# Kernel optimization log

Hardware: AMD Instinct MI355X
Metric: run time of the kernel (lower is better)

Reference implementation:

```python
import jax, jax.numpy as jnp
import numpy as np

N_NODES = 50000
N_EDGES = 800000
D_IN = 128
D_OUT = 128


def setup_inputs() -> dict:
    key = jax.random.key(0)
    k1, k2, k3, k4, k5, k6 = jax.random.split(key, 6)
    x = jax.random.normal(k1, (N_NODES, D_IN), dtype=jnp.float32)
    weight = jax.random.normal(k2, (D_IN, D_OUT), dtype=jnp.float32)
    bias = jax.random.normal(k3, (D_OUT,), dtype=jnp.float32)
    adj_row = jax.random.randint(k4, (N_EDGES,), 0, N_NODES, dtype=jnp.int64)
    adj_col = jax.random.randint(k5, (N_EDGES,), 0, N_NODES, dtype=jnp.int64)
    adj_val = jax.random.uniform(k6, (N_EDGES,), dtype=jnp.float32)
    return {"x": x, "weight": weight, "bias": bias,
            "adj_row": adj_row, "adj_col": adj_col, "adj_val": adj_val}


def reference(x, weight, bias, adj_row, adj_col, adj_val):
    # support = x @ W  -- dense GEMM [N, D_in] x [D_in, D_out]
    support = jnp.matmul(x, weight)
    # spmm(adj, support): out[i] = sum_e adj_val[e] * support[adj_col[e]] for adj_row[e]==i
    messages = support[adj_col] * adj_val[:, None]          # [E, D_out]
    output = jax.ops.segment_sum(messages, adj_row, num_segments=x.shape[0])
    return output + bias
```

## Files before the change

kernel.cpp:

```cpp
#include <hip/hip_runtime.h>

#define D 128
#define RPB 64
#define RPB_SHIFT 6
#define EPT 8
#define CHUNK (256 * EPT)
#define PASS_EDGES 1280

typedef __attribute__((ext_vector_type(8))) short short8;
typedef __attribute__((ext_vector_type(4))) float floatx4;
typedef __attribute__((ext_vector_type(4))) float f32x4;
typedef __attribute__((ext_vector_type(2))) unsigned int u32x2;
typedef unsigned int uint;
typedef unsigned short ushort;

__device__ inline short f2bf(float f) {
  unsigned u = __float_as_uint(f);
  u += 0x7FFF + ((u >> 16) & 1);
  return (short)(u >> 16);
}

__global__ __launch_bounds__(256) void hist_wconv_kernel(
    const int* __restrict__ adj_row, int* __restrict__ counts,
    int n_edges, int nb, int nc,
    const float* __restrict__ w, ushort* __restrict__ wt) {
  __shared__ int hist[1024];
  const int tid = threadIdx.x;

  if ((int)blockIdx.x < nc) {
    const int c = blockIdx.x;
    for (int i = tid; i < nb; i += 256) hist[i] = 0;
    __syncthreads();
    const int base = c * CHUNK + tid * EPT;
    if (base + EPT <= n_edges) {
      int4 r0 = *(const int4*)&adj_row[base];
      int4 r1 = *(const int4*)&adj_row[base + 4];
      int rr[EPT] = {r0.x, r0.y, r0.z, r0.w, r1.x, r1.y, r1.z, r1.w};
#pragma unroll
      for (int u = 0; u < EPT; ++u) atomicAdd(&hist[rr[u] >> RPB_SHIFT], 1);
    } else {
      for (int u = 0; u < EPT; ++u) {
        int e = base + u;
        if (e < n_edges) atomicAdd(&hist[adj_row[e] >> RPB_SHIFT], 1);
      }
    }
    __syncthreads();
    for (int b = tid; b < nb; b += 256)
      counts[(size_t)b * nc + c] = hist[b];
  } else {
    const int idx = ((int)blockIdx.x - nc) * 256 + tid;
    const int m = idx >> 4;
    const int ks = (idx & 15) * 8;
    short8 frag;
#pragma unroll
    for (int j = 0; j < 8; ++j) frag[j] = f2bf(w[(ks + j) * D + m]);
    *(short8*)&wt[(size_t)m * D + ks] = frag;
  }
}

__global__ __launch_bounds__(256) void scan_chunks_kernel(int* __restrict__ counts,
                                                          int* __restrict__ tot,
                                                          int nb, int nc) {
  __shared__ int buf[512];
  const int b = blockIdx.x;
  const int t = threadIdx.x;
  int v0 = (t < nc) ? counts[(size_t)b * nc + t] : 0;
  int v1 = (256 + t < nc) ? counts[(size_t)b * nc + 256 + t] : 0;
  buf[t] = v0;
  buf[256 + t] = v1;
  __syncthreads();
  for (int off = 1; off < 512; off <<= 1) {
    int a0 = buf[t], a1 = buf[256 + t];
    int d0 = (t >= off) ? buf[t - off] : 0;
    int d1 = (256 + t >= off) ? buf[256 + t - off] : 0;
    __syncthreads();
    buf[t] = a0 + d0;
    buf[256 + t] = a1 + d1;
    __syncthreads();
  }
  if (t < nc) counts[(size_t)b * nc + t] = buf[t] - v0;
  if (256 + t < nc) counts[(size_t)b * nc + 256 + t] = buf[256 + t] - v1;
  if (t == 0) tot[b] = buf[511];
}

__global__ __launch_bounds__(256) void scan_bins_kernel(const int* __restrict__ tot,
                                                        int* __restrict__ binStart,
                                                        int nb) {
  __shared__ int buf[1024];
  const int t = threadIdx.x;
  for (int i = t; i < 1024; i += 256) buf[i] = (i < nb) ? tot[i] : 0;
  __syncthreads();
  for (int off = 1; off < 1024; off <<= 1) {
    int a[4], d[4];
#pragma unroll
    for (int k = 0; k < 4; ++k) {
      int i = t + 256 * k;
      a[k] = buf[i];
      d[k] = (i >= off) ? buf[i - off] : 0;
    }
    __syncthreads();
#pragma unroll
    for (int k = 0; k < 4; ++k) buf[t + 256 * k] = a[k] + d[k];
    __syncthreads();
  }
  for (int i = t; i < nb; i += 256) binStart[i] = buf[i] - tot[i];
  if (t == 0) binStart[nb] = buf[1023];
}

__global__ __launch_bounds__(256) void gemm_sort_kernel(
    const float* __restrict__ x, const ushort* __restrict__ wt,
    ushort* __restrict__ support, int n_nodes, int gemm_blocks,
    const int* __restrict__ adj_row, const int* __restrict__ adj_col,
    const float* __restrict__ adj_val, const int* __restrict__ rel,
    const int* __restrict__ binStart, uint2* __restrict__ sorted,
    int n_edges, int nb, int nc) {
  __shared__ short sWA[2 * 8 * 64 * 8];
  const int tid = threadIdx.x;

  if ((int)blockIdx.x < gemm_blocks) {
    const int wid = tid >> 6;
    const int lane = tid & 63;
    const int quad = lane >> 4;
    const int node = blockIdx.x * 64 + wid * 16 + (lane & 15);
    const bool ok = (node < n_nodes);

    floatx4 acc[8];
#pragma unroll
    for (int mt = 0; mt < 8; ++mt) acc[mt] = (floatx4){0.f, 0.f, 0.f, 0.f};

#pragma unroll
    for (int kt2 = 0; kt2 < 4; kt2 += 2) {
      if (kt2) __syncthreads();
      for (int s = tid; s < 1024; s += 256) {
        int ktmt = s >> 6, ls = s & 63;
        int kt = kt2 + (ktmt >> 3);
        int kb = kt * 32 + (ls >> 4) * 8;
        int m = (ktmt & 7) * 16 + (ls & 15);
        *(short8*)&sWA[s * 8] = *(const short8*)&wt[(size_t)m * D + kb];
      }
      __syncthreads();

#pragma unroll
      for (int ktoff = 0; ktoff < 2; ++ktoff) {
        const int kt = kt2 + ktoff;
        short8 bfr = (short8){0, 0, 0, 0, 0, 0, 0, 0};
        if (ok) {
          const float4 v0 = *(const float4*)&x[(size_t)node * D + kt * 32 + quad * 8];
          const float4 v1 = *(const float4*)&x[(size_t)node * D + kt * 32 + quad * 8 + 4];
          bfr = (short8){f2bf(v0.x), f2bf(v0.y), f2bf(v0.z), f2bf(v0.w),
                         f2bf(v1.x), f2bf(v1.y), f2bf(v1.z), f2bf(v1.w)};
        }
#pragma unroll
        for (int mt = 0; mt < 8; ++mt) {
          short8 a = *(const short8*)&sWA[((ktoff * 8 + mt) * 64 + lane) * 8];
          acc[mt] = __builtin_amdgcn_mfma_f32_16x16x32_bf16(a, bfr, acc[mt], 0, 0, 0);
        }
      }
    }

    if (ok) {
#pragma unroll
      for (int mt = 0; mt < 8; ++mt) {
        uint lo = ((uint)(ushort)f2bf(acc[mt][1]) << 16) | (ushort)f2bf(acc[mt][0]);
        uint hi = ((uint)(ushort)f2bf(acc[mt][3]) << 16) | (ushort)f2bf(acc[mt][2]);
        *(uint2*)&support[(size_t)node * D + mt * 16 + quad * 4] = make_uint2(lo, hi);
      }
    }
  } else {
    int* loff = (int*)sWA;
    const int c = (int)blockIdx.x - gemm_blocks;
    for (int i = tid; i < nb; i += 256)
      loff[i] = binStart[i] + rel[(size_t)i * nc + c];
    __syncthreads();

    const int base = c * CHUNK + tid * EPT;
    if (base + EPT <= n_edges) {
      int4 r0 = *(const int4*)&adj_row[base];
      int4 r1 = *(const int4*)&adj_row[base + 4];
      int4 c0 = *(const int4*)&adj_col[base];
      int4 c1 = *(const int4*)&adj_col[base + 4];
      float4 v0 = *(const float4*)&adj_val[base];
      float4 v1 = *(const float4*)&adj_val[base + 4];
      int rr[EPT] = {r0.x, r0.y, r0.z, r0.w, r1.x, r1.y, r1.z, r1.w};
      int cc[EPT] = {c0.x, c0.y, c0.z, c0.w, c1.x, c1.y, c1.z, c1.w};
      float vv[EPT] = {v0.x, v0.y, v0.z, v0.w, v1.x, v1.y, v1.z, v1.w};
#pragma unroll
      for (int u = 0; u < EPT; ++u) {
        int r = rr[u];
        int pos = atomicAdd(&loff[r >> RPB_SHIFT], 1);
        sorted[pos] = make_uint2(((uint)(r & (RPB - 1)) << 16) | (uint)cc[u],
                                 __float_as_uint(vv[u]));
      }
    } else {
      for (int u = 0; u < EPT; ++u) {
        int e = base + u;
        if (e >= n_edges) break;
        int r = adj_row[e];
        int pos = atomicAdd(&loff[r >> RPB_SHIFT], 1);
        sorted[pos] = make_uint2(((uint)(r & (RPB - 1)) << 16) | (uint)adj_col[e],
                                 __float_as_uint(adj_val[e]));
      }
    }
  }
}

#define FMA8(vv, sv, IT)                                                  \
  do {                                                                    \
    acc[IT][0] = fmaf(vv, __uint_as_float((sv).x << 16), acc[IT][0]);     \
    acc[IT][1] = fmaf(vv, __uint_as_float((sv).x & 0xffff0000u), acc[IT][1]); \
    acc[IT][2] = fmaf(vv, __uint_as_float((sv).y << 16), acc[IT][2]);     \
    acc[IT][3] = fmaf(vv, __uint_as_float((sv).y & 0xffff0000u), acc[IT][3]); \
    acc[IT][4] = fmaf(vv, __uint_as_float((sv).z << 16), acc[IT][4]);     \
    acc[IT][5] = fmaf(vv, __uint_as_float((sv).z & 0xffff0000u), acc[IT][5]); \
    acc[IT][6] = fmaf(vv, __uint_as_float((sv).w << 16), acc[IT][6]);     \
    acc[IT][7] = fmaf(vv, __uint_as_float((sv).w & 0xffff0000u), acc[IT][7]); \
  } while (0)

__global__ __launch_bounds__(256) void bin_spmm_kernel(
    const uint2* __restrict__ sorted, const int* __restrict__ binStart,
    const uint* __restrict__ sup, const float* __restrict__ bias,
    float* __restrict__ out, int n_nodes) {
  __shared__ uint2 ebuf[PASS_EDGES];
  __shared__ int rowStart[RPB + 1];
  __shared__ int cursor[RPB];
  const int b = blockIdx.x;
  const int t = threadIdx.x;
  const int wid = t >> 6;
  const int lane = t & 63;
  const int qtr = lane >> 4;
  const int hl = lane & 15;

  const int s0 = binStart[b], s1 = binStart[b + 1];

  float acc[4][8];
#pragma unroll
  for (int it = 0; it < 4; ++it)
#pragma unroll
    for (int k = 0; k < 8; ++k) acc[it][k] = 0.f;

  for (int p0 = s0; p0 < s1; p0 += PASS_EDGES) {
    const int cntp = min(PASS_EDGES, s1 - p0);
    __syncthreads();
    if (t < RPB) cursor[t] = 0;
    __syncthreads();

    u32x2 er[8];
    int rr[8];
    const int base = p0 + t * EPT;
#pragma unroll
    for (int u = 0; u < EPT; ++u) {
      if (t * EPT + u < cntp) {
        er[u] = __builtin_nontemporal_load(
            (const u32x2*)&sorted[base + u]);
        rr[u] = (int)(er[u][0] >> 16);
        atomicAdd(&cursor[rr[u]], 1);
      } else {
        er[u] = (u32x2){0u, 0u};
        rr[u] = -1;
      }
    }
    __syncthreads();

    if (wid == 0) {
      int v = cursor[lane];
      int inc = v;
#pragma unroll
      for (int off = 1; off < 64; off <<= 1) {
        int u = __shfl_up(inc, off);
        if (lane >= off) inc += u;
      }
      rowStart[lane] = inc - v;
      if (lane == 63) rowStart[RPB] = inc;
    }
    __syncthreads();
    if (t < RPB) cursor[t] = rowStart[t];
    __syncthreads();

#pragma unroll
    for (int u = 0; u < EPT; ++u) {
      if (rr[u] >= 0) {
        int pos = atomicAdd(&cursor[rr[u]], 1);
        ebuf[pos] = make_uint2(er[u][0] & 0xFFFFu, er[u][1]);
      }
    }
    __syncthreads();

#pragma unroll
    for (int it = 0; it < 4; ++it) {
      const int rid = it * 16 + wid * 4 + qtr;
      const int js = rowStart[rid], je = rowStart[rid + 1];
      int j = js;
      for (; j + 8 <= je; j += 8) {
        uint cols[8];
        float vs[8];
#pragma unroll
        for (int u = 0; u < 8; ++u) {
          uint2 e = ebuf[j + u];
          cols[u] = e.x;
          vs[u] = __uint_as_float(e.y);
        }
        uint4 sv[8];
#pragma unroll
        for (int u = 0; u < 8; ++u)
          sv[u] = *(const uint4*)&sup[(size_t)cols[u] * 64 + hl * 4];
#pragma unroll
        for (int u = 0; u < 8; ++u) FMA8(vs[u], sv[u], it);
      }
      for (; j + 4 <= je; j += 4) {
        uint cols[4];
        float vs[4];
#pragma unroll
        for (int u = 0; u < 4; ++u) {
          uint2 e = ebuf[j + u];
          cols[u] = e.x;
          vs[u] = __uint_as_float(e.y);
        }
        uint4 sv[4];
#pragma unroll
        for (int u = 0; u < 4; ++u)
          sv[u] = *(const uint4*)&sup[(size_t)cols[u] * 64 + hl * 4];
#pragma unroll
        for (int u = 0; u < 4; ++u) FMA8(vs[u], sv[u], it);
      }
      for (; j < je; ++j) {
        uint2 e = ebuf[j];
        uint4 sv = *(const uint4*)&sup[(size_t)e.x * 64 + hl * 4];
        float v = __uint_as_float(e.y);
        FMA8(v, sv, it);
      }
    }
  }

  float4 b0 = *(const float4*)&bias[hl * 8];
  float4 b1 = *(const float4*)&bias[hl * 8 + 4];
#pragma unroll
  for (int it = 0; it < 4; ++it) {
    const int rid = it * 16 + wid * 4 + qtr;
    const int row = b * RPB + rid;
    if (row < n_nodes) {
      f32x4 o0 = {acc[it][0] + b0.x, acc[it][1] + b0.y,
                  acc[it][2] + b0.z, acc[it][3] + b0.w};
      f32x4 o1 = {acc[it][4] + b1.x, acc[it][5] + b1.y,
                  acc[it][6] + b1.z, acc[it][7] + b1.w};
      __builtin_nontemporal_store(o0, (f32x4*)&out[(size_t)row * D + hl * 8]);
      __builtin_nontemporal_store(o1, (f32x4*)&out[(size_t)row * D + hl * 8 + 4]);
    }
  }
}

extern "C" void kernel_launch(void* const* d_in, const int* in_sizes, int n_in,
                              void* d_out, int out_size, void* d_ws, size_t ws_size,
                              hipStream_t stream) {
  const float* x       = (const float*)d_in[0];
  const float* w       = (const float*)d_in[1];
  const float* bias    = (const float*)d_in[2];
  const int*   adj_row = (const int*)d_in[3];
  const int*   adj_col = (const int*)d_in[4];
  const float* adj_val = (const float*)d_in[5];

  const int n_nodes = in_sizes[0] / D;
  const int n_edges = in_sizes[3];
  float* out = (float*)d_out;

  const int nb = (n_nodes + RPB - 1) / RPB;
  const int nc = (n_edges + CHUNK - 1) / CHUNK;
  const int gemm_blocks = (n_nodes + 63) / 64;

  char* ws = (char*)d_ws;
  ushort* support  = (ushort*)ws; ws += ((size_t)n_nodes * D * 2 + 15) & ~15ull;
  int*    counts   = (int*)ws;    ws += ((size_t)nb * nc * 4 + 15) & ~15ull;
  int*    tot      = (int*)ws;    ws += ((size_t)nb * 4 + 15) & ~15ull;
  int*    binStart = (int*)ws;    ws += ((size_t)(nb + 1) * 4 + 15) & ~15ull;
  ushort* wt       = (ushort*)ws; ws += (size_t)D * D * 2;
  uint2*  sorted   = (uint2*)ws;  ws += (size_t)n_edges * 8;

  hist_wconv_kernel<<<nc + 8, 256, 0, stream>>>(adj_row, counts, n_edges, nb, nc,
                                                w, wt);

  scan_chunks_kernel<<<nb, 256, 0, stream>>>(counts, tot, nb, nc);

  scan_bins_kernel<<<1, 256, 0, stream>>>(tot, binStart, nb);

  gemm_sort_kernel<<<gemm_blocks + nc, 256, 0, stream>>>(
      x, wt, support, n_nodes, gemm_blocks,
      adj_row, adj_col, adj_val, counts, binStart, sorted, n_edges, nb, nc);

  bin_spmm_kernel<<<nb, 256, 0, stream>>>(sorted, binStart, (const uint*)support,
                                          bias, out, n_nodes);
}
```

Baseline: 142.4 us.

## Fuse bin scan into chunk scan via last-block atomic; load full W tile once

Removes the separate single-block scan_bins launch by having the last finishing scan_chunks block, detected with an atomic counter plus thread fences, perform the bin-total scan. The counter is reset inside the histogram kernel. The GEMM path now stages all four K-slices of the bf16 weight into shared memory in one pass, dropping the intermediate __syncthreads. This doubles LDS use per block, which may lower occupancy. The change trades one kernel launch for fence and atomic overhead.

```diff
diff --git a/kernel.cpp b/kernel.cpp
--- a/kernel.cpp
+++ b/kernel.cpp
@@ -6,6 +6,7 @@
 #define EPT 8
 #define CHUNK (256 * EPT)
 #define PASS_EDGES 1280
+#define NBMAX 1024
 
 typedef __attribute__((ext_vector_type(8))) short short8;
 typedef __attribute__((ext_vector_type(4))) float floatx4;
@@ -23,8 +24,9 @@
 __global__ __launch_bounds__(256) void hist_wconv_kernel(
     const int* __restrict__ adj_row, int* __restrict__ counts,
     int n_edges, int nb, int nc,
-    const float* __restrict__ w, ushort* __restrict__ wt) {
-  __shared__ int hist[1024];
+    const float* __restrict__ w, ushort* __restrict__ wt,
+    int* __restrict__ scanflag) {
+  __shared__ int hist[NBMAX];
   const int tid = threadIdx.x;
 
   if ((int)blockIdx.x < nc) {
@@ -49,6 +51,7 @@
       counts[(size_t)b * nc + c] = hist[b];
   } else {
     const int idx = ((int)blockIdx.x - nc) * 256 + tid;
+    if (idx == 0) *scanflag = 0;
     const int m = idx >> 4;
     const int ks = (idx & 15) * 8;
     short8 frag;
@@ -58,10 +61,12 @@
   }
 }
 
-__global__ __launch_bounds__(256) void scan_chunks_kernel(int* __restrict__ counts,
-                                                          int* __restrict__ tot,
-                                                          int nb, int nc) {
-  __shared__ int buf[512];
+__global__ __launch_bounds__(256) void scan_chunks_kernel(
+    int* __restrict__ counts, int* __restrict__ tot,
+    int* __restrict__ binStart, int* __restrict__ scanflag,
+    int nb, int nc) {
+  __shared__ int buf[NBMAX];
+  __shared__ int amLast;
   const int b = blockIdx.x;
   const int t = threadIdx.x;
   int v0 = (t < nc) ? counts[(size_t)b * nc + t] : 0;
@@ -81,16 +86,17 @@
   if (t < nc) counts[(size_t)b * nc + t] = buf[t] - v0;
   if (256 + t < nc) counts[(size_t)b * nc + 256 + t] = buf[256 + t] - v1;
   if (t == 0) tot[b] = buf[511];
-}
-
-__global__ __launch_bounds__(256) void scan_bins_kernel(const int* __restrict__ tot,
-                                                        int* __restrict__ binStart,
-                                                        int nb) {
-  __shared__ int buf[1024];
-  const int t = threadIdx.x;
-  for (int i = t; i < 1024; i += 256) buf[i] = (i < nb) ? tot[i] : 0;
+
+  __threadfence();
   __syncthreads();
-  for (int off = 1; off < 1024; off <<= 1) {
+  if (t == 0) amLast = (atomicAdd(scanflag, 1) == nb - 1);
+  __syncthreads();
+  if (!amLast) return;
+  __threadfence();
+
+  for (int i = t; i < NBMAX; i += 256) buf[i] = (i < nb) ? tot[i] : 0;
+  __syncthreads();
+  for (int off = 1; off < NBMAX; off <<= 1) {
     int a[4], d[4];
 #pragma unroll
     for (int k = 0; k < 4; ++k) {
@@ -104,7 +110,7 @@
     __syncthreads();
   }
   for (int i = t; i < nb; i += 256) binStart[i] = buf[i] - tot[i];
-  if (t == 0) binStart[nb] = buf[1023];
+  if (t == 0) binStart[nb] = buf[NBMAX - 1];
 }
 
 __global__ __launch_bounds__(256) void gemm_sort_kernel(
@@ -114,7 +120,7 @@
     const float* __restrict__ adj_val, const int* __restrict__ rel,
     const int* __restrict__ binStart, uint2* __restrict__ sorted,
     int n_edges, int nb, int nc) {
-  __shared__ short sWA[2 * 8 * 64 * 8];
+  __shared__ short sWA[4 * 8 * 64 * 8];
   const int tid = threadIdx.x;
 
   if ((int)blockIdx.x < gemm_blocks) {
@@ -128,33 +134,28 @@
 #pragma unroll
     for (int mt = 0; mt < 8; ++mt) acc[mt] = (floatx4){0.f, 0.f, 0.f, 0.f};
 
-#pragma unroll
-    for (int kt2 = 0; kt2 < 4; kt2 += 2) {
-      if (kt2) __syncthreads();
-      for (int s = tid; s < 1024; s += 256) {
-        int ktmt = s >> 6, ls = s & 63;
-        int kt = kt2 + (ktmt >> 3);
-        int kb = kt * 32 + (ls >> 4) * 8;
-        int m = (ktmt & 7) * 16 + (ls & 15);
-        *(short8*)&sWA[s * 8] = *(const short8*)&wt[(size_t)m * D + kb];
-      }
-      __syncthreads();
-
-#pragma unroll
-      for (int ktoff = 0; ktoff < 2; ++ktoff) {
-        const int kt = kt2 + ktoff;
-        short8 bfr = (short8){0, 0, 0, 0, 0, 0, 0, 0};
-        if (ok) {
-          const float4 v0 = *(const float4*)&x[(size_t)node * D + kt * 32 + quad * 8];
-          const float4 v1 = *(const float4*)&x[(size_t)node * D + kt * 32 + quad * 8 + 4];
-          bfr = (short8){f2bf(v0.x), f2bf(v0.y), f2bf(v0.z), f2bf(v0.w),
-                         f2bf(v1.x), f2bf(v1.y), f2bf(v1.z), f2bf(v1.w)};
-        }
-#pragma unroll
-        for (int mt = 0; mt < 8; ++mt) {
-          short8 a = *(const short8*)&sWA[((ktoff * 8 + mt) * 64 + lane) * 8];
-          acc[mt] = __builtin_amdgcn_mfma_f32_16x16x32_bf16(a, bfr, acc[mt], 0, 0, 0);
-        }
+    for (int s = tid; s < 2048; s += 256) {
+      int ktmt = s >> 6, ls = s & 63;
+      int kt = ktmt >> 3;
+      int kb = kt * 32 + (ls >> 4) * 8;
+      int m = (ktmt & 7) * 16 + (ls & 15);
+      *(short8*)&sWA[s * 8] = *(const short8*)&wt[(size_t)m * D + kb];
+    }
+    __syncthreads();
+
+#pragma unroll
+    for (int kt = 0; kt < 4; ++kt) {
+      short8 bfr = (short8){0, 0, 0, 0, 0, 0, 0, 0};
+      if (ok) {
+        const float4 v0 = *(const float4*)&x[(size_t)node * D + kt * 32 + quad * 8];
+        const float4 v1 = *(const float4*)&x[(size_t)node * D + kt * 32 + quad * 8 + 4];
+        bfr = (short8){f2bf(v0.x), f2bf(v0.y), f2bf(v0.z), f2bf(v0.w),
+                       f2bf(v1.x), f2bf(v1.y), f2bf(v1.z), f2bf(v1.w)};
+      }
+#pragma unroll
+      for (int mt = 0; mt < 8; ++mt) {
+        short8 a = *(const short8*)&sWA[((kt * 8 + mt) * 64 + lane) * 8];
+        acc[mt] = __builtin_amdgcn_mfma_f32_16x16x32_bf16(a, bfr, acc[mt], 0, 0, 0);
       }
     }
 
@@ -372,14 +373,14 @@
   int*    tot      = (int*)ws;    ws += ((size_t)nb * 4 + 15) & ~15ull;
   int*    binStart = (int*)ws;    ws += ((size_t)(nb + 1) * 4 + 15) & ~15ull;
   ushort* wt       = (ushort*)ws; ws += (size_t)D * D * 2;
+  int*    scanflag = (int*)ws;    ws += 16;
   uint2*  sorted   = (uint2*)ws;  ws += (size_t)n_edges * 8;
 
   hist_wconv_kernel<<<nc + 8, 256, 0, stream>>>(adj_row, counts, n_edges, nb, nc,
-                                                w, wt);
-
-  scan_chunks_kernel<<<nb, 256, 0, stream>>>(counts, tot, nb, nc);
-
-  scan_bins_kernel<<<1, 256, 0, stream>>>(tot, binStart, nb);
+                                                w, wt, scanflag);
+
+  scan_chunks_kernel<<<nb, 256, 0, stream>>>(counts, tot, binStart, scanflag,
+                                             nb, nc);
 
   gemm_sort_kernel<<<gemm_blocks + nc, 256, 0, stream>>>(
       x, wt, support, n_nodes, gemm_blocks,
```

Result: slower. 200.0 us (+40.5%).
